# Kernel optimization log

Hardware: AMD Instinct MI355X
Metric: run time of the kernel (lower is better)

## Reference

```python
import jax, jax.numpy as jnp
import numpy as np

K = 3          # kernel_size
PAD = K // 2   # unfold padding
BN_EPS = 1e-5


def _conv(x, w, dilation, pad):
    # x: [B,C,H,W], w: [O,I,kh,kw]
    return jax.lax.conv_general_dilated(
        x, w, window_strides=(1, 1), padding=[(pad, pad), (pad, pad)],
        rhs_dilation=(dilation, dilation),
        dimension_numbers=("NCHW", "OIHW", "NCHW"))


def _bn(x, g, b, rm, rv):
    # eval-mode batchnorm with running stats
    inv = g / jnp.sqrt(rv + BN_EPS)
    return x * inv[None, :, None, None] + (b - rm * inv)[None, :, None, None]


def setup_inputs() -> dict:
    key = jax.random.key(0)
    ks = jax.random.split(key, 8)
    B, T, H, W = 8, 5, 512, 512
    mid = 16  # max(16, T // 4)
    inp = {
        "x_aligned": jax.random.normal(ks[0], (B, T, H, W), jnp.float32),
        "raw_diff": jax.random.normal(ks[1], (B, T - 1, H, W), jnp.float32),
        "w1": jax.random.normal(ks[2], (mid, T, 3, 3), jnp.float32) * 0.1,
        "g1": jnp.ones((mid,), jnp.float32), "b1": jnp.zeros((mid,), jnp.float32),
        "rm1": jnp.zeros((mid,), jnp.float32), "rv1": jnp.ones((mid,), jnp.float32),
        "w2": jax.random.normal(ks[3], (mid, mid, 3, 3), jnp.float32) * 0.1,
        "g2": jnp.ones((mid,), jnp.float32), "b2": jnp.zeros((mid,), jnp.float32),
        "rm2": jnp.zeros((mid,), jnp.float32), "rv2": jnp.ones((mid,), jnp.float32),
        "w3": jax.random.normal(ks[4], (mid, mid, 3, 3), jnp.float32) * 0.1,
        "g3": jnp.ones((mid,), jnp.float32), "b3": jnp.zeros((mid,), jnp.float32),
        "rm3": jnp.zeros((mid,), jnp.float32), "rv3": jnp.ones((mid,), jnp.float32),
        "w4": jax.random.normal(ks[5], (T * K * K, mid, 1, 1), jnp.float32) * 0.1,
        "bias": jnp.full((1,), -1.0, jnp.float32),
    }
    return inp


def reference(x_aligned, raw_diff, w1, g1, b1, rm1, rv1, w2, g2, b2, rm2, rv2,
              w3, g3, b3, rm3, rv3, w4, bias):
    B, T, H, W = x_aligned.shape
    # _accumulate: sequential abs-add == sum of abs over frame-diff axis
    acc = jnp.sum(jnp.abs(raw_diff), axis=1, keepdims=True)  # [B,1,H,W]
    mean = jnp.mean(acc)
    n = acc.size
    std = jnp.sqrt(jnp.sum((acc - mean) ** 2) / (n - 1))  # unbiased (torch default)
    motion = (acc - mean) / (std + 1e-6)
    motion_seq = jnp.broadcast_to(motion, (B, T, H, W))
    # _generate_kernel: conv+BN+ReLU stack with dilations 1,2,4 then 1x1
    h = jax.nn.relu(_bn(_conv(motion_seq, w1, 1, 1), g1, b1, rm1, rv1))
    h = jax.nn.relu(_bn(_conv(h, w2, 2, 2), g2, b2, rm2, rv2))
    h = jax.nn.relu(_bn(_conv(h, w3, 4, 4), g3, b3, rm3, rv3))
    raw_kernel = _conv(h, w4, 1, 0).reshape(B, T, K * K, H, W)
    kernel = (jax.nn.sigmoid(raw_kernel + bias[0]) + 0.01) * 10.0
    # _enhance: unfold (KxK patches, zero pad) then per-pixel weighted sum
    xp = jnp.pad(x_aligned, ((0, 0), (0, 0), (PAD, PAD), (PAD, PAD)))
    patches = jnp.stack(
        [xp[:, :, i:i + H, j:j + W] for i in range(K) for j in range(K)],
        axis=2)  # [B,T,K*K,H,W], matches F.unfold row-major kernel order
    return jnp.sum(kernel * patches, axis=2)  # [B,T,H,W]
```

## Files before the change

kernel.cpp:

```cpp
#include <hip/hip_runtime.h>
#include <hip/hip_bf16.h>
#include <math.h>

#define HH 512
#define WW 512
#define BB 8
#define TT 5
#define MID 16
#define HWSZ (HH*WW)
#define NPIX (BB*HWSZ)

typedef __attribute__((ext_vector_type(8))) short bf16x8;
typedef __attribute__((ext_vector_type(4))) short bf16x4;
typedef __attribute__((ext_vector_type(4))) float f32x4;

#if __has_builtin(__builtin_amdgcn_exp2f)
#define EXP2F(x) __builtin_amdgcn_exp2f(x)
#else
#define EXP2F(x) exp2f(x)
#endif

#define LOG2E 1.4426950408889634f

__device__ inline unsigned short f2bf(float f){
  unsigned u = __float_as_uint(f);
  u = u + 0x7fffu + ((u >> 16) & 1u);
  return (unsigned short)(u >> 16);
}
__device__ inline unsigned packpair(float a, float b){
  unsigned ua = __float_as_uint(a) + 0x8000u;
  unsigned ub = __float_as_uint(b) + 0x8000u;
  return __builtin_amdgcn_perm(ub, ua, 0x07060302u);
}
__device__ inline float blo(unsigned u){ return __uint_as_float(u << 16); }
__device__ inline float bhi(unsigned u){ return __uint_as_float(u & 0xffff0000u); }

union U4B { uint4 u; bf16x8 h; };
union U2B { uint2 u; bf16x4 h; };


__global__ __launch_bounds__(256) void k_acc(const float* __restrict__ rd,
    float4* __restrict__ acc, float2* __restrict__ partial,
    const float* __restrict__ w1, const float* __restrict__ g1, const float* __restrict__ b1,
    const float* __restrict__ rm1, const float* __restrict__ rv1,
    const float* __restrict__ w2, const float* __restrict__ g2, const float* __restrict__ b2,
    const float* __restrict__ rm2, const float* __restrict__ rv2,
    const float* __restrict__ w3, const float* __restrict__ g3, const float* __restrict__ b3,
    const float* __restrict__ rm3, const float* __restrict__ rv3,
    const float* __restrict__ w4, const float* __restrict__ bias0,
    float* __restrict__ cst, uint2* __restrict__ wsA1,
    unsigned* __restrict__ wsB2, unsigned* __restrict__ wsB3, uint2* __restrict__ wsB4){
  int t = threadIdx.x;
  if (blockIdx.x == 2048){
    if (t == 0) cst[242] = bias0[0] * LOG2E;
    if (t < 16){
      float s1 = g1[t] * rsqrtf(rv1[t] + 1e-5f);
      cst[162 + t] = b1[t] - rm1[t] * s1;
      float c2 = g2[t] * rsqrtf(rv2[t] + 1e-5f);
      cst[288 + t] = c2; cst[304 + t] = b2[t] - rm2[t] * c2;
      float c3 = g3[t] * rsqrtf(rv3[t] + 1e-5f);
      cst[320 + t] = c3; cst[336 + t] = b3[t] - rm3[t] * c3;
    }
    if (t < 64){
      int o = t & 15, qq = t >> 4;
      float s1o = g1[o] * rsqrtf(rv1[o] + 1e-5f);
      unsigned pk2[2];
      #pragma unroll
      for (int h = 0; h < 2; h++){
        unsigned lo = 0, hi = 0;
        int tp0 = qq*4 + 2*h, tp1 = tp0 + 1;
        if (tp0 < 9){ float sw = 0.f; for (int f = 0; f < TT; f++) sw += w1[o*45 + f*9 + tp0]; lo = f2bf(sw * s1o); }
        if (tp1 < 9){ float sw = 0.f; for (int f = 0; f < TT; f++) sw += w1[o*45 + f*9 + tp1]; hi = f2bf(sw * s1o); }
        pk2[h] = lo | (hi << 16);
      }
      wsA1[t] = make_uint2(pk2[0], pk2[1]);
    }
    for (int it = 0; it < 5; it++){
      int idx = it * 256 + t;
      int m = idx >> 8, rem = idx & 255;
      int L = rem >> 2, jj = rem & 3;
      int out = L & 15, q = L >> 4;
      unsigned v2 = 0, v3 = 0;
      #pragma unroll
      for (int h = 0; h < 2; h++){
        int j = 2*jj + h;
        int k = q*8 + j;
        int tap = 2*m + (k >> 4);
        int ci = k & 15;
        unsigned bv2 = 0, bv3 = 0;
        if (tap < 9){
          bv2 = f2bf(w2[out*144 + ci*9 + tap]);
          bv3 = f2bf(w3[out*144 + ci*9 + tap]);
        }
        v2 |= bv2 << (16*h);
        v3 |= bv3 << (16*h);
      }
      wsB2[idx] = v2; wsB3[idx] = v3;
    }
    if (t < 192){
      int c = t >> 6, L = t & 63;
      int n = L & 15, q = L >> 4;
      int o = c*16 + n;
      unsigned pk0 = 0, pk1 = 0;
      if (o < 45){
        unsigned b0 = f2bf(w4[o*16 + q*4 + 0] * LOG2E);
        unsigned b1v = f2bf(w4[o*16 + q*4 + 1] * LOG2E);
        unsigned b2v = f2bf(w4[o*16 + q*4 + 2] * LOG2E);
        unsigned b3v = f2bf(w4[o*16 + q*4 + 3] * LOG2E);
        pk0 = b0 | (b1v << 16);
        pk1 = b2v | (b3v << 16);
      }
      wsB4[c*64 + L] = make_uint2(pk0, pk1);
    }
    return;
  }
  int gt = blockIdx.x * 256 + t;
  int i = gt << 2;
  int b = i >> 18, p = i & (HWSZ - 1);
  const float* base = rd + (size_t)b * 4 * HWSZ + p;
  float4 f0 = *(const float4*)(base);
  float4 f1 = *(const float4*)(base + HWSZ);
  float4 f2 = *(const float4*)(base + 2*HWSZ);
  float4 f3 = *(const float4*)(base + 3*HWSZ);
  float4 s4;
  s4.x = fabsf(f0.x) + fabsf(f1.x) + fabsf(f2.x) + fabsf(f3.x);
  s4.y = fabsf(f0.y) + fabsf(f1.y) + fabsf(f2.y) + fabsf(f3.y);
  s4.z = fabsf(f0.z) + fabsf(f1.z) + fabsf(f2.z) + fabsf(f3.z);
  s4.w = fabsf(f0.w) + fabsf(f1.w) + fabsf(f2.w) + fabsf(f3.w);
  acc[gt] = s4;
  float s  = s4.x + s4.y + s4.z + s4.w;
  float s2 = s4.x*s4.x + s4.y*s4.y + s4.z*s4.z + s4.w*s4.w;
  #pragma unroll
  for (int off = 32; off; off >>= 1){
    s  += __shfl_down(s,  off);
    s2 += __shfl_down(s2, off);
  }
  __shared__ float ls[4], ls2[4];
  int lane = t & 63, wid = t >> 6;
  if (lane == 0){ ls[wid] = s; ls2[wid] = s2; }
  __syncthreads();
  if (t == 0)
    partial[blockIdx.x] = make_float2(ls[0]+ls[1]+ls[2]+ls[3],
                                      ls2[0]+ls2[1]+ls2[2]+ls2[3]);
}

#define TR 12
#define TC 68
__global__ __launch_bounds__(256) void k_conv12(const float* __restrict__ acc,
                                                const float2* __restrict__ partial,
                                                const float* __restrict__ C,
                                                const uint2* __restrict__ wsA1,
                                                const unsigned* __restrict__ wsB2,
                                                uint2* __restrict__ h2){
  __shared__ struct {
    float AT[14*72];
    uint4 PLq[816*2];
  } SM;
  __shared__ float rs[4], rs2[4];
  int tid = threadIdx.x;
  int blk = blockIdx.x;
  int xt = blk & 7, yt = (blk >> 3) & 63, b = blk >> 9;
  int y0 = yt << 3, x0 = xt << 6;

  float s = 0.f, s2 = 0.f;
  for (int j = tid; j < 1024; j += 256){
    float4 v = ((const float4*)partial)[j];
    s += v.x + v.z; s2 += v.y + v.w;
  }
  #pragma unroll
  for (int off = 32; off; off >>= 1){
    s  += __shfl_down(s,  off);
    s2 += __shfl_down(s2, off);
  }
  if ((tid & 63) == 0){ rs[tid >> 6] = s; rs2[tid >> 6] = s2; }
  __syncthreads();
  float S  = rs[0] + rs[1] + rs[2] + rs[3];
  float S2 = rs2[0] + rs2[1] + rs2[2] + rs2[3];
  float n = (float)NPIX;
  float mean = S / n;
  float var  = (S2 - n * mean * mean) / (n - 1.0f);
  float inv  = 1.f / (sqrtf(var) + 1e-6f);

  const float* ab = acc + ((size_t)b << 18);
  #pragma unroll
  for (int it = 0; it < 4; it++){
    int idx = it*256 + tid;
    if (idx < 14*72){
      int r = (idx * 1821) >> 17;
      int p = idx - r*72;
      int gy = y0 - 3 + r, gx = x0 - 3 + p;
      float v = 0.f;
      if ((unsigned)gy < HH && (unsigned)gx < WW)
        v = (ab[(gy << 9) + gx] - mean) * inv;
      SM.AT[idx] = v;
    }
  }
  __syncthreads();

  int lane = tid & 63, wv = tid >> 6;
  int col = lane & 15, q = lane >> 4;

  {
    U2B a1; a1.u = wsA1[lane];
    float4 b1v = *(const float4*)&C[162 + q*4];
    f32x4 cinit = {b1v.x, b1v.y, b1v.z, b1v.w};
    int off_[4];
    #pragma unroll
    for (int j = 0; j < 4; j++){
      int tap = q*4 + j;
      int ky = (tap*11) >> 5;
      int kx = tap - 3*ky;
      off_[j] = (ky*72 + kx)*4;
    }
    const char* ATb = (const char*)SM.AT;
    char* PLb = (char*)SM.PLq;
    for (int tt = wv; tt < 51; tt += 4){
      int p = tt*16 + col;
      int r2 = (p * 241) >> 14;
      int p2 = p - r2*TC;
      int bofs = (r2*72 + p2) * 4;
      float m0 = *(const float*)(ATb + bofs + off_[0]);
      float m1 = *(const float*)(ATb + bofs + off_[1]);
      float m2 = *(const float*)(ATb + bofs + off_[2]);
      float m3 = *(const float*)(ATb + bofs + off_[3]);
      U2B bfr;
      bfr.u.x = packpair(m0, m1);
      bfr.u.y = packpair(m2, m3);
      f32x4 z = __builtin_amdgcn_mfma_f32_16x16x16bf16_1k(a1.h, bfr.h, cinit, 0, 0, 0);
      int gy = y0 - 2 + r2, gx = x0 - 2 + p2;
      unsigned pk0 = 0u, pk1 = 0u;
      if (((unsigned)gy < HH) && ((unsigned)gx < WW)){
        pk0 = packpair(fmaxf(0.f, z[0]), fmaxf(0.f, z[1]));
        pk1 = packpair(fmaxf(0.f, z[2]), fmaxf(0.f, z[3]));
      }
      *(uint2*)(PLb + p*32 + q*8) = make_uint2(pk0, pk1);
    }
  }
  __syncthreads();

  int chSel = q & 1;
  bool hiTap = (q >= 2);
  uint4 wfrag[5];
  #pragma unroll
  for (int m = 0; m < 5; m++) wfrag[m] = ((const uint4*)wsB2)[m*64 + lane];
  float4 sc = *(const float4*)&C[288 + q*4];
  float4 bi = *(const float4*)&C[304 + q*4];
  #pragma unroll
  for (int rr = 0; rr < 2; rr++){
    int ly = wv*2 + rr;
    #pragma unroll
    for (int g = 0; g < 4; g++){
      int lx = g << 4;
      f32x4 cc = {0.f, 0.f, 0.f, 0.f};
      #pragma unroll
      for (int m = 0; m < 5; m++){
        const int ta = 2*m, tb = (2*m + 1 > 8) ? 8 : (2*m + 1);
        int dy = (hiTap ? tb/3 : ta/3) - 1;
        int dx = (hiTap ? tb%3 : ta%3) - 1;
        int trow = ly + 2 + 2*dy;
        int tpx  = lx + 2 + col + 2*dx;
        U4B bv; bv.u = SM.PLq[(unsigned)((trow*TC + tpx) << 1) | (unsigned)chSel];
        U4B wb; wb.u = wfrag[m];
        cc = __builtin_amdgcn_mfma_f32_16x16x32_bf16(wb.h, bv.h, cc, 0, 0, 0);
      }
      float v0 = fmaxf(0.f, fmaf(cc[0], sc.x, bi.x));
      float v1 = fmaxf(0.f, fmaf(cc[1], sc.y, bi.y));
      float v2 = fmaxf(0.f, fmaf(cc[2], sc.z, bi.z));
      float v3 = fmaxf(0.f, fmaf(cc[3], sc.w, bi.w));
      int gy = y0 + ly, gx = x0 + lx + col;
      h2[(size_t)((b << 18) | (gy << 9) | gx)*4 + q] =
          make_uint2(packpair(v0, v1), packpair(v2, v3));
    }
  }
}

template<bool EDGE>
__device__ inline f32x4 convW4(const uint4* __restrict__ hin, const uint4 wfrag[5],
                               int b, int y, int x0, int col, int q, f32x4 cc){
  int chSel = q & 1;
  bool hiTap = (q >= 2);
  #pragma unroll
  for (int m = 0; m < 5; m++){
    const int ta = 2*m, tb = (2*m + 1 > 8) ? 8 : (2*m + 1);
    int dy = (hiTap ? tb/3 : ta/3) - 1;
    int dx = (hiTap ? tb%3 : ta%3) - 1;
    int yy = y + dy * 4;
    int xx = x0 + col + dx * 4;
    U4B a;
    if (EDGE){
      bool valid = ((unsigned)yy < HH) && ((unsigned)xx < WW);
      a.u = make_uint4(0u, 0u, 0u, 0u);
      if (valid) a.u = hin[(((unsigned)((b << 18) | (yy << 9) | xx)) << 1) | (unsigned)chSel];
    } else {
      a.u = hin[(((unsigned)((b << 18) | (yy << 9) | xx)) << 1) | (unsigned)chSel];
    }
    U4B bb; bb.u = wfrag[m];
    cc = __builtin_amdgcn_mfma_f32_16x16x32_bf16(bb.h, a.h, cc, 0, 0, 0);
  }
  return cc;
}

__device__ __forceinline__ void stage2_tail(int g, f32x4 cc, float4 sc, float4 bi,
    float cb, const uint2 bw4[3], char* myL, int q, int col){
  float v0 = fmaxf(0.f, fmaf(cc[0], sc.x, bi.x));
  float v1 = fmaxf(0.f, fmaf(cc[1], sc.y, bi.y));
  float v2 = fmaxf(0.f, fmaf(cc[2], sc.z, bi.z));
  float v3 = fmaxf(0.f, fmaf(cc[3], sc.w, bi.w));
  U2B bb;
  bb.u.x = packpair(v0, v1);
  bb.u.y = packpair(v2, v3);
  char* wp = myL + (g*16 + col)*104 + q*8;
  #pragma unroll
  for (int c = 0; c < 3; c++){
    f32x4 aw = {cb, cb, cb, cb};
    U2B af; af.u = bw4[c];
    aw = __builtin_amdgcn_mfma_f32_16x16x16bf16_1k(af.h, bb.h, aw, 0, 0, 0);
    float k0 = fmaf(10.f, __builtin_amdgcn_rcpf(1.f + EXP2F(-aw[0])), 0.1f);
    float k1 = fmaf(10.f, __builtin_amdgcn_rcpf(1.f + EXP2F(-aw[1])), 0.1f);
    float k2 = fmaf(10.f, __builtin_amdgcn_rcpf(1.f + EXP2F(-aw[2])), 0.1f);
    float k3 = fmaf(10.f, __builtin_amdgcn_rcpf(1.f + EXP2F(-aw[3])), 0.1f);
    *(uint2*)(wp + c*32) = make_uint2(packpair(k0, k1), packpair(k2, k3));
  }
}

__global__ __launch_bounds__(256, 3) void k_conv3m(const uint4* __restrict__ h2,
                                                   const float* __restrict__ C,
                                                   const unsigned* __restrict__ wsB3,
                                                   const uint2* __restrict__ wsB4,
                                                   const float* __restrict__ xal,
                                                   float* __restrict__ out){
  __shared__ uint2 LB[4][832];
  int lane = threadIdx.x & 63, wv = threadIdx.x >> 6;
  char* myL = (char*)LB[wv];
  int w = blockIdx.x * 4 + wv;
  int base = w << 6;
  int b = base >> 18, rem = base & (HWSZ - 1);
  int y = rem >> 9, wx = rem & 511;
  uint4 wfrag[5];
  #pragma unroll
  for (int m = 0; m < 5; m++) wfrag[m] = ((const uint4*)wsB3)[m*64 + lane];
  uint2 bw4[3];
  #pragma unroll
  for (int c = 0; c < 3; c++) bw4[c] = wsB4[c*64 + lane];
  int col = lane & 15, q = lane >> 4;
  int chSel = q & 1;
  bool hiTap = (q >= 2);
  float4 sc = *(const float4*)&C[320 + q*4];
  float4 bi = *(const float4*)&C[336 + q*4];
  float cb = C[242];

  bool f1 = (y >= 4) && (y < 508) && (wx >= 64) && (wx <= 384);
  if (f1){
    const int dyA[5] = {-1,-1,0,1,1}, dyB[5] = {-1,0,0,1,1};
    const int dxA[5] = {-1,1,0,-1,1}, dxB[5] = {0,-1,1,0,1};
    const char* hb = (const char*)h2
        + ((((size_t)b << 18) + (unsigned)(y << 9)) << 5)
        + ((unsigned)(wx + col) << 5) + (chSel << 4);
    const char* pmt[5];
    #pragma unroll
    for (int m = 0; m < 5; m++){
      int off = hiTap ? (dyB[m]*65536 + dxB[m]*128)
                      : (dyA[m]*65536 + dxA[m]*128);
      pmt[m] = hb + off;
    }
    uint4 tap[4][5];
    #pragma unroll
    for (int g = 0; g < 4; g++){
      #pragma unroll
      for (int m = 0; m < 5; m++)
        tap[g][m] = *(const uint4*)(pmt[m] + g*512);
    }
    #pragma unroll
    for (int g = 0; g < 4; g++){
      f32x4 cc = {0.f, 0.f, 0.f, 0.f};
      #pragma unroll
      for (int m = 0; m < 5; m++){
        U4B bv; bv.u = tap[g][m];
        U4B wb; wb.u = wfrag[m];
        cc = __builtin_amdgcn_mfma_f32_16x16x32_bf16(wb.h, bv.h, cc, 0, 0, 0);
      }
      stage2_tail(g, cc, sc, bi, cb, bw4, myL, q, col);
    }
  } else {
    bool yIn = (y >= 4) && (y < 508);
    #pragma unroll
    for (int g = 0; g < 4; g++){
      int x0 = wx + g*16;
      f32x4 cc = {0.f, 0.f, 0.f, 0.f};
      bool fast = yIn && (x0 >= 4) && (x0 <= 492);
      if (fast) cc = convW4<false>(h2, wfrag, b, y, x0, col, q, cc);
      else      cc = convW4<true >(h2, wfrag, b, y, x0, col, q, cc);
      stage2_tail(g, cc, sc, bi, cb, bw4, myL, q, col);
    }
  }

  unsigned kvf[24];
  {
    const uint2* kp = (const uint2*)(myL + lane*104);
    #pragma unroll
    for (int jj = 0; jj < 12; jj++){
      uint2 u = kp[jj];
      kvf[2*jj] = u.x; kvf[2*jj+1] = u.y;
    }
  }
  int px = wx + lane;
  bool f3 = (y > 0) && (y < 511) && (wx != 0) && (wx != 448);
  if (f3){
    const char* p0 = (const char*)xal + (((size_t)(b*TT)) << 20)
                   + (unsigned)(y << 11) + (px << 2);
    #pragma unroll
    for (int t = 0; t < TT; t++){
      const char* pc = p0 + (size_t)t * (HWSZ*4);
      float xv[9];
      xv[0] = *(const float*)(pc - 2052);
      xv[1] = *(const float*)(pc - 2048);
      xv[2] = *(const float*)(pc - 2044);
      xv[3] = *(const float*)(pc - 4);
      xv[4] = *(const float*)(pc);
      xv[5] = *(const float*)(pc + 4);
      xv[6] = *(const float*)(pc + 2044);
      xv[7] = *(const float*)(pc + 2048);
      xv[8] = *(const float*)(pc + 2052);
      float ov = 0.f;
      #pragma unroll
      for (int k = 0; k < 9; k++){
        int n = t*9 + k;
        unsigned u = kvf[n >> 1];
        float kf = (n & 1) ? bhi(u) : blo(u);
        ov = fmaf(kf, xv[k], ov);
      }
      out[((size_t)(b*TT + t) << 18) + (y << 9) + px] = ov;
    }
  } else {
    bool mxl = (px > 0), mxr = (px < 511), mym = (y > 0), myp = (y < 511);
    bool msk[9] = { mym&&mxl, mym, mym&&mxr,
                    mxl,      true, mxr,
                    myp&&mxl, myp, myp&&mxr };
    int rowm = mym ? -2048 : 0;
    int rowp = myp ?  2048 : 0;
    int loff = mxl ? -4 : 0;
    int roff = mxr ?  4 : 0;
    const char* base0 = (const char*)(xal + ((size_t)(b*TT) << 18) + (y << 9) + px);
    #pragma unroll
    for (int t = 0; t < TT; t++){
      const char* pc = base0 + (size_t)t * (HWSZ*4);
      const char* pm = pc + rowm;
      const char* pp = pc + rowp;
      float xv[9];
      xv[0] = *(const float*)(pm + loff);
      xv[1] = *(const float*)(pm);
      xv[2] = *(const float*)(pm + roff);
      xv[3] = *(const float*)(pc + loff);
      xv[4] = *(const float*)(pc);
      xv[5] = *(const float*)(pc + roff);
      xv[6] = *(const float*)(pp + loff);
      xv[7] = *(const float*)(pp);
      xv[8] = *(const float*)(pp + roff);
      float ov = 0.f;
      #pragma unroll
      for (int k = 0; k < 9; k++){
        int n = t*9 + k;
        unsigned u = kvf[n >> 1];
        float kf = (n & 1) ? bhi(u) : blo(u);
        float kern = msk[k] ? kf : 0.f;
        ov = fmaf(kern, xv[k], ov);
      }
      out[((size_t)(b*TT + t) << 18) + (y << 9) + px] = ov;
    }
  }
}

extern "C" void kernel_launch(void* const* d_in, const int* in_sizes, int n_in,
                              void* d_out, int out_size, void* d_ws, size_t ws_size,
                              hipStream_t stream){
  const float* xal = (const float*)d_in[0];
  const float* rd  = (const float*)d_in[1];
  const float* w1  = (const float*)d_in[2];
  const float* g1  = (const float*)d_in[3];
  const float* b1  = (const float*)d_in[4];
  const float* rm1 = (const float*)d_in[5];
  const float* rv1 = (const float*)d_in[6];
  const float* w2  = (const float*)d_in[7];
  const float* g2  = (const float*)d_in[8];
  const float* b2  = (const float*)d_in[9];
  const float* rm2 = (const float*)d_in[10];
  const float* rv2 = (const float*)d_in[11];
  const float* w3  = (const float*)d_in[12];
  const float* g3  = (const float*)d_in[13];
  const float* b3  = (const float*)d_in[14];
  const float* rm3 = (const float*)d_in[15];
  const float* rv3 = (const float*)d_in[16];
  const float* w4  = (const float*)d_in[17];
  const float* bias= (const float*)d_in[18];
  float* out = (float*)d_out;

  char* ws = (char*)d_ws;
  float2*   partial = (float2*)ws;
  float*    cst   = (float*)(ws + 16384);
  unsigned* wsB2  = (unsigned*)(ws + 32768);
  unsigned* wsB3  = (unsigned*)(ws + 40960);
  uint2*    wsB4  = (uint2*)(ws + 49152);
  uint2*    wsA1  = (uint2*)(ws + 57344);
  float*    acc   = (float*)(ws + 65536);
  char*     h2    = (char*)(ws + 65536 + (size_t)NPIX*4);

  k_acc<<<2049, 256, 0, stream>>>(rd, (float4*)acc, partial,
                                  w1, g1, b1, rm1, rv1,
                                  w2, g2, b2, rm2, rv2,
                                  w3, g3, b3, rm3, rv3,
                                  w4, bias, cst, wsA1, wsB2, wsB3, wsB4);
  k_conv12<<<4096, 256, 0, stream>>>(acc, partial, cst, wsA1, wsB2, (uint2*)h2);
  k_conv3m<<<NPIX/256, 256, 0, stream>>>((const uint4*)h2, cst, wsB3, wsB4, xal, out);
}
```

Baseline: 242.8 us.

## Fuse conv1-3 and enhancement into one halo-tiled kernel, dropping h2 global buffer

Merges the conv1+conv2 kernel and the conv3+1x1+enhance kernel into a single 512-thread kernel working on 16x32 pixel tiles. The tile carries a 7-pixel halo so all three dilated convolutions run from LDS, and the intermediate h2 activation no longer makes a round trip through global memory. The x_aligned loads are issued before the conv3 MFMA phase to hide their latency, and the per-wave kernel-weight scratch uses an XOR swizzle with a 96-byte stride to avoid bank conflicts. The cost is heavy halo recomputation of conv1 and conv2 (44x44 and 40x40 regions for a 32x16 output tile), plus large LDS use and register pressure that may cut occupancy.

Result: no change. 243.9 us (+0.4%).

```diff
diff --git a/kernel.cpp b/kernel.cpp
--- a/kernel.cpp
+++ b/kernel.cpp
@@ -144,163 +144,7 @@
                                       ls2[0]+ls2[1]+ls2[2]+ls2[3]);
 }
 
-#define TR 12
-#define TC 68
-__global__ __launch_bounds__(256) void k_conv12(const float* __restrict__ acc,
-                                                const float2* __restrict__ partial,
-                                                const float* __restrict__ C,
-                                                const uint2* __restrict__ wsA1,
-                                                const unsigned* __restrict__ wsB2,
-                                                uint2* __restrict__ h2){
-  __shared__ struct {
-    float AT[14*72];
-    uint4 PLq[816*2];
-  } SM;
-  __shared__ float rs[4], rs2[4];
-  int tid = threadIdx.x;
-  int blk = blockIdx.x;
-  int xt = blk & 7, yt = (blk >> 3) & 63, b = blk >> 9;
-  int y0 = yt << 3, x0 = xt << 6;
-
-  float s = 0.f, s2 = 0.f;
-  for (int j = tid; j < 1024; j += 256){
-    float4 v = ((const float4*)partial)[j];
-    s += v.x + v.z; s2 += v.y + v.w;
-  }
-  #pragma unroll
-  for (int off = 32; off; off >>= 1){
-    s  += __shfl_down(s,  off);
-    s2 += __shfl_down(s2, off);
-  }
-  if ((tid & 63) == 0){ rs[tid >> 6] = s; rs2[tid >> 6] = s2; }
-  __syncthreads();
-  float S  = rs[0] + rs[1] + rs[2] + rs[3];
-  float S2 = rs2[0] + rs2[1] + rs2[2] + rs2[3];
-  float n = (float)NPIX;
-  float mean = S / n;
-  float var  = (S2 - n * mean * mean) / (n - 1.0f);
-  float inv  = 1.f / (sqrtf(var) + 1e-6f);
-
-  const float* ab = acc + ((size_t)b << 18);
-  #pragma unroll
-  for (int it = 0; it < 4; it++){
-    int idx = it*256 + tid;
-    if (idx < 14*72){
-      int r = (idx * 1821) >> 17;
-      int p = idx - r*72;
-      int gy = y0 - 3 + r, gx = x0 - 3 + p;
-      float v = 0.f;
-      if ((unsigned)gy < HH && (unsigned)gx < WW)
-        v = (ab[(gy << 9) + gx] - mean) * inv;
-      SM.AT[idx] = v;
-    }
-  }
-  __syncthreads();
-
-  int lane = tid & 63, wv = tid >> 6;
-  int col = lane & 15, q = lane >> 4;
-
-  {
-    U2B a1; a1.u = wsA1[lane];
-    float4 b1v = *(const float4*)&C[162 + q*4];
-    f32x4 cinit = {b1v.x, b1v.y, b1v.z, b1v.w};
-    int off_[4];
-    #pragma unroll
-    for (int j = 0; j < 4; j++){
-      int tap = q*4 + j;
-      int ky = (tap*11) >> 5;
-      int kx = tap - 3*ky;
-      off_[j] = (ky*72 + kx)*4;
-    }
-    const char* ATb = (const char*)SM.AT;
-    char* PLb = (char*)SM.PLq;
-    for (int tt = wv; tt < 51; tt += 4){
-      int p = tt*16 + col;
-      int r2 = (p * 241) >> 14;
-      int p2 = p - r2*TC;
-      int bofs = (r2*72 + p2) * 4;
-      float m0 = *(const float*)(ATb + bofs + off_[0]);
-      float m1 = *(const float*)(ATb + bofs + off_[1]);
-      float m2 = *(const float*)(ATb + bofs + off_[2]);
-      float m3 = *(const float*)(ATb + bofs + off_[3]);
-      U2B bfr;
-      bfr.u.x = packpair(m0, m1);
-      bfr.u.y = packpair(m2, m3);
-      f32x4 z = __builtin_amdgcn_mfma_f32_16x16x16bf16_1k(a1.h, bfr.h, cinit, 0, 0, 0);
-      int gy = y0 - 2 + r2, gx = x0 - 2 + p2;
-      unsigned pk0 = 0u, pk1 = 0u;
-      if (((unsigned)gy < HH) && ((unsigned)gx < WW)){
-        pk0 = packpair(fmaxf(0.f, z[0]), fmaxf(0.f, z[1]));
-        pk1 = packpair(fmaxf(0.f, z[2]), fmaxf(0.f, z[3]));
-      }
-      *(uint2*)(PLb + p*32 + q*8) = make_uint2(pk0, pk1);
-    }
-  }
-  __syncthreads();
-
-  int chSel = q & 1;
-  bool hiTap = (q >= 2);
-  uint4 wfrag[5];
-  #pragma unroll
-  for (int m = 0; m < 5; m++) wfrag[m] = ((const uint4*)wsB2)[m*64 + lane];
-  float4 sc = *(const float4*)&C[288 + q*4];
-  float4 bi = *(const float4*)&C[304 + q*4];
-  #pragma unroll
-  for (int rr = 0; rr < 2; rr++){
-    int ly = wv*2 + rr;
-    #pragma unroll
-    for (int g = 0; g < 4; g++){
-      int lx = g << 4;
-      f32x4 cc = {0.f, 0.f, 0.f, 0.f};
-      #pragma unroll
-      for (int m = 0; m < 5; m++){
-        const int ta = 2*m, tb = (2*m + 1 > 8) ? 8 : (2*m + 1);
-        int dy = (hiTap ? tb/3 : ta/3) - 1;
-        int dx = (hiTap ? tb%3 : ta%3) - 1;
-        int trow = ly + 2 + 2*dy;
-        int tpx  = lx + 2 + col + 2*dx;
-        U4B bv; bv.u = SM.PLq[(unsigned)((trow*TC + tpx) << 1) | (unsigned)chSel];
-        U4B wb; wb.u = wfrag[m];
-        cc = __builtin_amdgcn_mfma_f32_16x16x32_bf16(wb.h, bv.h, cc, 0, 0, 0);
-      }
-      float v0 = fmaxf(0.f, fmaf(cc[0], sc.x, bi.x));
-      float v1 = fmaxf(0.f, fmaf(cc[1], sc.y, bi.y));
-      float v2 = fmaxf(0.f, fmaf(cc[2], sc.z, bi.z));
-      float v3 = fmaxf(0.f, fmaf(cc[3], sc.w, bi.w));
-      int gy = y0 + ly, gx = x0 + lx + col;
-      h2[(size_t)((b << 18) | (gy << 9) | gx)*4 + q] =
-          make_uint2(packpair(v0, v1), packpair(v2, v3));
-    }
-  }
-}
-
-template<bool EDGE>
-__device__ inline f32x4 convW4(const uint4* __restrict__ hin, const uint4 wfrag[5],
-                               int b, int y, int x0, int col, int q, f32x4 cc){
-  int chSel = q & 1;
-  bool hiTap = (q >= 2);
-  #pragma unroll
-  for (int m = 0; m < 5; m++){
-    const int ta = 2*m, tb = (2*m + 1 > 8) ? 8 : (2*m + 1);
-    int dy = (hiTap ? tb/3 : ta/3) - 1;
-    int dx = (hiTap ? tb%3 : ta%3) - 1;
-    int yy = y + dy * 4;
-    int xx = x0 + col + dx * 4;
-    U4B a;
-    if (EDGE){
-      bool valid = ((unsigned)yy < HH) && ((unsigned)xx < WW);
-      a.u = make_uint4(0u, 0u, 0u, 0u);
-      if (valid) a.u = hin[(((unsigned)((b << 18) | (yy << 9) | xx)) << 1) | (unsigned)chSel];
-    } else {
-      a.u = hin[(((unsigned)((b << 18) | (yy << 9) | xx)) << 1) | (unsigned)chSel];
-    }
-    U4B bb; bb.u = wfrag[m];
-    cc = __builtin_amdgcn_mfma_f32_16x16x32_bf16(bb.h, a.h, cc, 0, 0, 0);
-  }
-  return cc;
-}
-
-__device__ __forceinline__ void stage2_tail(int g, f32x4 cc, float4 sc, float4 bi,
+__device__ __forceinline__ void stage2_tail96(int g, f32x4 cc, float4 sc, float4 bi,
     float cb, const uint2 bw4[3], char* myL, int q, int col){
   float v0 = fmaxf(0.f, fmaf(cc[0], sc.x, bi.x));
   float v1 = fmaxf(0.f, fmaf(cc[1], sc.y, bi.y));
@@ -309,7 +153,8 @@
   U2B bb;
   bb.u.x = packpair(v0, v1);
   bb.u.y = packpair(v2, v3);
-  char* wp = myL + (g*16 + col)*104 + q*8;
+  int px = g*16 + col;
+  char* wp = myL + px*96 + ((q ^ ((px >> 2) & 3)) << 3);
   #pragma unroll
   for (int c = 0; c < 3; c++){
     f32x4 aw = {cb, cb, cb, cb};
@@ -323,113 +168,241 @@
   }
 }
 
-__global__ __launch_bounds__(256, 3) void k_conv3m(const uint4* __restrict__ h2,
-                                                   const float* __restrict__ C,
-                                                   const unsigned* __restrict__ wsB3,
-                                                   const uint2* __restrict__ wsB4,
-                                                   const float* __restrict__ xal,
-                                                   float* __restrict__ out){
-  __shared__ uint2 LB[4][832];
-  int lane = threadIdx.x & 63, wv = threadIdx.x >> 6;
-  char* myL = (char*)LB[wv];
-  int w = blockIdx.x * 4 + wv;
-  int base = w << 6;
-  int b = base >> 18, rem = base & (HWSZ - 1);
-  int y = rem >> 9, wx = rem & 511;
-  uint4 wfrag[5];
-  #pragma unroll
-  for (int m = 0; m < 5; m++) wfrag[m] = ((const uint4*)wsB3)[m*64 + lane];
-  uint2 bw4[3];
-  #pragma unroll
-  for (int c = 0; c < 3; c++) bw4[c] = wsB4[c*64 + lane];
+__global__ __launch_bounds__(512, 4) void k_fuse(const float* __restrict__ acc,
+    const float2* __restrict__ partial, const float* __restrict__ C,
+    const uint2* __restrict__ wsA1, const unsigned* __restrict__ wsB2,
+    const unsigned* __restrict__ wsB3, const uint2* __restrict__ wsB4,
+    const float* __restrict__ xal, float* __restrict__ out){
+  __shared__ uint4 LDSQ[5120];
+  char* lds = (char*)LDSQ;
+  char* h2b = lds;
+  char* h1b = lds + 30720;
+  float* ATf = (float*)(lds + 70144);
+  float* rsf = (float*)lds;
+
+  int tid = threadIdx.x;
+  int lane = tid & 63, wv = tid >> 6;
+  int blk = blockIdx.x;
+  int tx0 = (blk & 15) << 5;
+  int ty0 = ((blk >> 4) & 31) << 4;
+  int b = blk >> 9;
+
+  float s = 0.f, s2 = 0.f;
+  #pragma unroll
+  for (int j = 0; j < 2; j++){
+    float4 v = ((const float4*)partial)[j*512 + tid];
+    s += v.x + v.z; s2 += v.y + v.w;
+  }
+  #pragma unroll
+  for (int off = 32; off; off >>= 1){
+    s  += __shfl_down(s,  off);
+    s2 += __shfl_down(s2, off);
+  }
+  if (lane == 0){ rsf[wv] = s; rsf[8 + wv] = s2; }
+  __syncthreads();
+  float S = 0.f, S2 = 0.f;
+  #pragma unroll
+  for (int c = 0; c < 8; c++){ S += rsf[c]; S2 += rsf[8 + c]; }
+  float n = (float)NPIX;
+  float mean = S / n;
+  float var  = (S2 - n * mean * mean) / (n - 1.0f);
+  float inv  = 1.f / (sqrtf(var) + 1e-6f);
+
+  const float* ab = acc + ((size_t)b << 18);
+  #pragma unroll
+  for (int it = 0; it < 3; it++){
+    int idx = it*512 + tid;
+    if (idx < 1380){
+      int r = (idx * 5699) >> 18;
+      int p = idx - r*46;
+      int gy = ty0 - 7 + r, gx = tx0 - 7 + p;
+      float v = 0.f;
+      if ((unsigned)gy < HH && (unsigned)gx < WW)
+        v = (ab[(gy << 9) + gx] - mean) * inv;
+      ATf[idx] = v;
+    } else if (idx < 1520){
+      ATf[idx] = 0.f;
+    }
+  }
+  __syncthreads();
+
   int col = lane & 15, q = lane >> 4;
   int chSel = q & 1;
   bool hiTap = (q >= 2);
-  float4 sc = *(const float4*)&C[320 + q*4];
-  float4 bi = *(const float4*)&C[336 + q*4];
-  float cb = C[242];
-
-  bool f1 = (y >= 4) && (y < 508) && (wx >= 64) && (wx <= 384);
-  if (f1){
-    const int dyA[5] = {-1,-1,0,1,1}, dyB[5] = {-1,0,0,1,1};
-    const int dxA[5] = {-1,1,0,-1,1}, dxB[5] = {0,-1,1,0,1};
-    const char* hb = (const char*)h2
-        + ((((size_t)b << 18) + (unsigned)(y << 9)) << 5)
-        + ((unsigned)(wx + col) << 5) + (chSel << 4);
-    const char* pmt[5];
-    #pragma unroll
-    for (int m = 0; m < 5; m++){
-      int off = hiTap ? (dyB[m]*65536 + dxB[m]*128)
-                      : (dyA[m]*65536 + dxA[m]*128);
-      pmt[m] = hb + off;
-    }
-    uint4 tap[4][5];
-    #pragma unroll
-    for (int g = 0; g < 4; g++){
-      #pragma unroll
-      for (int m = 0; m < 5; m++)
-        tap[g][m] = *(const uint4*)(pmt[m] + g*512);
-    }
-    #pragma unroll
-    for (int g = 0; g < 4; g++){
+
+  {
+    U2B a1; a1.u = wsA1[lane];
+    float4 b1v = *(const float4*)&C[162 + q*4];
+    f32x4 cinit = {b1v.x, b1v.y, b1v.z, b1v.w};
+    int off_[4];
+    #pragma unroll
+    for (int j = 0; j < 4; j++){
+      int tap = q*4 + j;
+      int ky = (tap*11) >> 5;
+      int kx = tap - 3*ky;
+      off_[j] = (ky*46 + kx)*4;
+    }
+    const char* ATb = (const char*)ATf;
+    for (int tt = wv; tt < 77; tt += 8){
+      int p = tt*16 + col;
+      int r2 = (p * 5958) >> 18;
+      int p2 = p - r2*44;
+      int bofs = (r2*46 + p2)*4;
+      float m0 = *(const float*)(ATb + bofs + off_[0]);
+      float m1 = *(const float*)(ATb + bofs + off_[1]);
+      float m2 = *(const float*)(ATb + bofs + off_[2]);
+      float m3 = *(const float*)(ATb + bofs + off_[3]);
+      U2B bfr;
+      bfr.u.x = packpair(m0, m1);
+      bfr.u.y = packpair(m2, m3);
+      f32x4 z = __builtin_amdgcn_mfma_f32_16x16x16bf16_1k(a1.h, bfr.h, cinit, 0, 0, 0);
+      int gy = ty0 + r2 - 6, gx = tx0 + p2 - 6;
+      unsigned pk0 = 0u, pk1 = 0u;
+      if (((unsigned)gy < HH) && ((unsigned)gx < WW)){
+        pk0 = packpair(fmaxf(0.f, z[0]), fmaxf(0.f, z[1]));
+        pk1 = packpair(fmaxf(0.f, z[2]), fmaxf(0.f, z[3]));
+      }
+      *(uint2*)(h1b + p*32 + q*8) = make_uint2(pk0, pk1);
+    }
+  }
+  __syncthreads();
+
+  {
+    uint4 wfrag[5];
+    #pragma unroll
+    for (int m = 0; m < 5; m++) wfrag[m] = ((const uint4*)wsB2)[m*64 + lane];
+    float4 sc = *(const float4*)&C[288 + q*4];
+    float4 bi = *(const float4*)&C[304 + q*4];
+    for (int tt = wv; tt < 60; tt += 8){
+      int p = tt*16 + col;
+      int r3 = (p * 6554) >> 18;
+      int p3 = p - r3*40;
+      const char* bb0 = h1b + (unsigned)((r3*44 + p3) << 5) + (chSel << 4);
       f32x4 cc = {0.f, 0.f, 0.f, 0.f};
       #pragma unroll
       for (int m = 0; m < 5; m++){
-        U4B bv; bv.u = tap[g][m];
+        const int ta = 2*m, tb = (2*m + 1 > 8) ? 8 : (2*m + 1);
+        int dy = (hiTap ? tb/3 : ta/3) - 1;
+        int dx = (hiTap ? tb%3 : ta%3) - 1;
+        int imm = (((2 + 2*dy)*44) + (2 + 2*dx)) << 5;
+        U4B bv; bv.u = *(const uint4*)(bb0 + imm);
         U4B wb; wb.u = wfrag[m];
         cc = __builtin_amdgcn_mfma_f32_16x16x32_bf16(wb.h, bv.h, cc, 0, 0, 0);
       }
-      stage2_tail(g, cc, sc, bi, cb, bw4, myL, q, col);
-    }
-  } else {
-    bool yIn = (y >= 4) && (y < 508);
-    #pragma unroll
-    for (int g = 0; g < 4; g++){
-      int x0 = wx + g*16;
-      f32x4 cc = {0.f, 0.f, 0.f, 0.f};
-      bool fast = yIn && (x0 >= 4) && (x0 <= 492);
-      if (fast) cc = convW4<false>(h2, wfrag, b, y, x0, col, q, cc);
-      else      cc = convW4<true >(h2, wfrag, b, y, x0, col, q, cc);
-      stage2_tail(g, cc, sc, bi, cb, bw4, myL, q, col);
-    }
+      float v0 = fmaxf(0.f, fmaf(cc[0], sc.x, bi.x));
+      float v1 = fmaxf(0.f, fmaf(cc[1], sc.y, bi.y));
+      float v2 = fmaxf(0.f, fmaf(cc[2], sc.z, bi.z));
+      float v3 = fmaxf(0.f, fmaf(cc[3], sc.w, bi.w));
+      int gy = ty0 + r3 - 4, gx = tx0 + p3 - 4;
+      unsigned pk0 = 0u, pk1 = 0u;
+      if (((unsigned)gy < HH) && ((unsigned)gx < WW)){
+        pk0 = packpair(v0, v1);
+        pk1 = packpair(v2, v3);
+      }
+      *(uint2*)(h2b + p*32 + q*8) = make_uint2(pk0, pk1);
+    }
+  }
+  __syncthreads();
+
+  uint4 wfrag3[5];
+  #pragma unroll
+  for (int m = 0; m < 5; m++) wfrag3[m] = ((const uint4*)wsB3)[m*64 + lane];
+  uint2 bw4[3];
+  #pragma unroll
+  for (int c = 0; c < 3; c++) bw4[c] = wsB4[c*64 + lane];
+  float4 sc3 = *(const float4*)&C[320 + q*4];
+  float4 bi3 = *(const float4*)&C[336 + q*4];
+  float cb = C[242];
+  char* myL = lds + 30720 + wv*6144;
+  int rbase = wv*2;
+  bool ySlow = (ty0 == 0 && wv == 0) || (ty0 == 496 && wv == 7);
+  int y  = ty0 + rbase + (lane >> 5);
+  int px = tx0 + (lane & 31);
+
+  float xv[TT][9];
+  if (!ySlow){
+    const char* p0 = (const char*)xal + (((size_t)(b*TT)) << 20)
+                   + (unsigned)(y << 11) + (px << 2);
+    #pragma unroll
+    for (int t = 0; t < TT; t++){
+      const char* pc = p0 + (size_t)t * (HWSZ*4);
+      xv[t][0] = *(const float*)(pc - 2052);
+      xv[t][1] = *(const float*)(pc - 2048);
+      xv[t][2] = *(const float*)(pc - 2044);
+      xv[t][3] = *(const float*)(pc - 4);
+      xv[t][4] = *(const float*)(pc);
+      xv[t][5] = *(const float*)(pc + 4);
+      xv[t][6] = *(const float*)(pc + 2044);
+      xv[t][7] = *(const float*)(pc + 2048);
+      xv[t][8] = *(const float*)(pc + 2052);
+    }
+  }
+
+  #pragma unroll
+  for (int g = 0; g < 4; g++){
+    int row = rbase + (g >> 1);
+    int x0 = (g & 1) << 4;
+    const char* bb0 = h2b + (unsigned)((row*40 + x0 + col) << 5) + (chSel << 4);
+    f32x4 cc = {0.f, 0.f, 0.f, 0.f};
+    #pragma unroll
+    for (int m = 0; m < 5; m++){
+      const int ta = 2*m, tb = (2*m + 1 > 8) ? 8 : (2*m + 1);
+      int dy = (hiTap ? tb/3 : ta/3) - 1;
+      int dx = (hiTap ? tb%3 : ta%3) - 1;
+      int imm = (((4 + 4*dy)*40) + (4 + 4*dx)) << 5;
+      U4B bv; bv.u = *(const uint4*)(bb0 + imm);
+      U4B wb; wb.u = wfrag3[m];
+      cc = __builtin_amdgcn_mfma_f32_16x16x32_bf16(wb.h, bv.h, cc, 0, 0, 0);
+    }
+    stage2_tail96(g, cc, sc3, bi3, cb, bw4, myL, q, col);
   }
 
   unsigned kvf[24];
   {
-    const uint2* kp = (const uint2*)(myL + lane*104);
-    #pragma unroll
-    for (int jj = 0; jj < 12; jj++){
-      uint2 u = kp[jj];
-      kvf[2*jj] = u.x; kvf[2*jj+1] = u.y;
-    }
-  }
-  int px = wx + lane;
-  bool f3 = (y > 0) && (y < 511) && (wx != 0) && (wx != 448);
-  if (f3){
-    const char* p0 = (const char*)xal + (((size_t)(b*TT)) << 20)
-                   + (unsigned)(y << 11) + (px << 2);
-    #pragma unroll
-    for (int t = 0; t < TT; t++){
-      const char* pc = p0 + (size_t)t * (HWSZ*4);
-      float xv[9];
-      xv[0] = *(const float*)(pc - 2052);
-      xv[1] = *(const float*)(pc - 2048);
-      xv[2] = *(const float*)(pc - 2044);
-      xv[3] = *(const float*)(pc - 4);
-      xv[4] = *(const float*)(pc);
-      xv[5] = *(const float*)(pc + 4);
-      xv[6] = *(const float*)(pc + 2044);
-      xv[7] = *(const float*)(pc + 2048);
-      xv[8] = *(const float*)(pc + 2052);
-      float ov = 0.f;
-      #pragma unroll
-      for (int k = 0; k < 9; k++){
-        int n = t*9 + k;
-        unsigned u = kvf[n >> 1];
-        float kf = (n & 1) ? bhi(u) : blo(u);
-        ov = fmaf(kf, xv[k], ov);
-      }
-      out[((size_t)(b*TT + t) << 18) + (y << 9) + px] = ov;
+    int k3 = (lane >> 2) & 3;
+    const char* kp = myL + lane*96;
+    #pragma unroll
+    for (int c = 0; c < 3; c++){
+      #pragma unroll
+      for (int qq = 0; qq < 4; qq++){
+        uint2 u = *(const uint2*)(kp + c*32 + ((qq ^ k3) << 3));
+        kvf[(c*4 + qq)*2]     = u.x;
+        kvf[(c*4 + qq)*2 + 1] = u.y;
+      }
+    }
+  }
+
+  if (!ySlow){
+    bool xe = (tx0 == 0) || (tx0 == 480);
+    if (xe){
+      bool mxl = (px > 0), mxr = (px < 511);
+      #pragma unroll
+      for (int t = 0; t < TT; t++){
+        float ov = 0.f;
+        #pragma unroll
+        for (int k = 0; k < 9; k++){
+          int nn = t*9 + k;
+          unsigned u = kvf[nn >> 1];
+          float kf = (nn & 1) ? bhi(u) : blo(u);
+          if (k % 3 == 0)      kf = mxl ? kf : 0.f;
+          else if (k % 3 == 2) kf = mxr ? kf : 0.f;
+          ov = fmaf(kf, xv[t][k], ov);
+        }
+        out[((size_t)(b*TT + t) << 18) + (y << 9) + px] = ov;
+      }
+    } else {
+      #pragma unroll
+      for (int t = 0; t < TT; t++){
+        float ov = 0.f;
+        #pragma unroll
+        for (int k = 0; k < 9; k++){
+          int nn = t*9 + k;
+          unsigned u = kvf[nn >> 1];
+          float kf = (nn & 1) ? bhi(u) : blo(u);
+          ov = fmaf(kf, xv[t][k], ov);
+        }
+        out[((size_t)(b*TT + t) << 18) + (y << 9) + px] = ov;
+      }
     }
   } else {
     bool mxl = (px > 0), mxr = (px < 511), mym = (y > 0), myp = (y < 511);
@@ -446,24 +419,24 @@
       const char* pc = base0 + (size_t)t * (HWSZ*4);
       const char* pm = pc + rowm;
       const char* pp = pc + rowp;
-      float xv[9];
-      xv[0] = *(const float*)(pm + loff);
-      xv[1] = *(const float*)(pm);
-      xv[2] = *(const float*)(pm + roff);
-      xv[3] = *(const float*)(pc + loff);
-      xv[4] = *(const float*)(pc);
-      xv[5] = *(const float*)(pc + roff);
-      xv[6] = *(const float*)(pp + loff);
-      xv[7] = *(const float*)(pp);
-      xv[8] = *(const float*)(pp + roff);
+      float zv[9];
+      zv[0] = *(const float*)(pm + loff);
+      zv[1] = *(const float*)(pm);
+      zv[2] = *(const float*)(pm + roff);
+      zv[3] = *(const float*)(pc + loff);
+      zv[4] = *(const float*)(pc);
+      zv[5] = *(const float*)(pc + roff);
+      zv[6] = *(const float*)(pp + loff);
+      zv[7] = *(const float*)(pp);
+      zv[8] = *(const float*)(pp + roff);
       float ov = 0.f;
       #pragma unroll
       for (int k = 0; k < 9; k++){
-        int n = t*9 + k;
-        unsigned u = kvf[n >> 1];
-        float kf = (n & 1) ? bhi(u) : blo(u);
+        int nn = t*9 + k;
+        unsigned u = kvf[nn >> 1];
+        float kf = (nn & 1) ? bhi(u) : blo(u);
         float kern = msk[k] ? kf : 0.f;
-        ov = fmaf(kern, xv[k], ov);
+        ov = fmaf(kern, zv[k], ov);
       }
       out[((size_t)(b*TT + t) << 18) + (y << 9) + px] = ov;
     }
@@ -502,13 +475,12 @@
   uint2*    wsB4  = (uint2*)(ws + 49152);
   uint2*    wsA1  = (uint2*)(ws + 57344);
   float*    acc   = (float*)(ws + 65536);
-  char*     h2    = (char*)(ws + 65536 + (size_t)NPIX*4);
 
   k_acc<<<2049, 256, 0, stream>>>(rd, (float4*)acc, partial,
                                   w1, g1, b1, rm1, rv1,
                                   w2, g2, b2, rm2, rv2,
                                   w3, g3, b3, rm3, rv3,
                                   w4, bias, cst, wsA1, wsB2, wsB3, wsB4);
-  k_conv12<<<4096, 256, 0, stream>>>(acc, partial, cst, wsA1, wsB2, (uint2*)h2);
-  k_conv3m<<<NPIX/256, 256, 0, stream>>>((const uint4*)h2, cst, wsB3, wsB4, xal, out);
-}
+  k_fuse<<<4096, 512, 0, stream>>>(acc, partial, cst, wsA1, wsB2, wsB3, wsB4,
+                                   xal, out);
+}
```
